# Kernel tuning notes

Hardware: AMD Instinct MI355X
Metric: run time of the kernel (lower is better)

The kernel has to match this reference:

```python
import jax, jax.numpy as jnp
import numpy as np

B, T, D = 2, 2048, 1024
K, F = 8, 4096
LAMBDA = 0.5


def setup_inputs() -> dict:
    key = jax.random.key(0)
    ks = jax.random.split(key, 8)
    s = 0.02
    return {
        "x": jax.random.normal(ks[0], (B, T, D), dtype=jnp.float32),
        "prev_logits": jax.random.normal(ks[1], (B, T, K), dtype=jnp.float32),
        "Wt": jax.random.normal(ks[2], (D, K), dtype=jnp.float32) * s,
        "Wgt": jax.random.normal(ks[3], (K, K), dtype=jnp.float32) * s,
        "We_logits": jnp.zeros((K,), dtype=jnp.float32),
        "W1": jax.random.normal(ks[4], (K, D, F), dtype=jnp.float32) * s,
        "b1": jnp.zeros((K, F), dtype=jnp.float32),
        "W2": jax.random.normal(ks[5], (K, F, D), dtype=jnp.float32) * s,
        "b2": jnp.zeros((K, D), dtype=jnp.float32),
    }


def reference(x, prev_logits, Wt, Wgt, We_logits, W1, b1, W2, b2):
    # gating: softmax over router logits, sigmoid-threshold multi-hot mask
    logits = jnp.einsum("btd,dk->btk", x, Wt) + jnp.einsum("btk,kj->btj", prev_logits, Wgt)
    st = jax.nn.softmax(logits, axis=-1)                       # (B,T,K)
    We = jax.nn.sigmoid(We_logits)                             # (K,)
    mask = (st > LAMBDA * We).astype(x.dtype)                  # (B,T,K)
    g = st * mask
    sel_counts = mask.sum(axis=(0, 1))                         # (K,)
    avg_density = mask.sum(axis=-1).mean()                     # scalar

    # dense multi-expert FFN: every expert on every token (dropout=0 / eval)
    h = jax.nn.gelu(jnp.einsum("btd,kdf->bktf", x, W1) + b1[:, None, :], approximate=False)
    outk = jnp.einsum("bktf,kfd->bktd", h, W2) + b2[:, None, :]  # (B,K,T,D)
    y = jnp.einsum("btk,bktd->btd", g, outk)
    y = y / (g.sum(axis=-1, keepdims=True) + 1e-6)
    return y, jax.lax.stop_gradient(logits), sel_counts, avg_density
```

## Files before the change

### kernel.cpp

```cpp
#include <hip/hip_runtime.h>
#include <cstdint>
#include <cstddef>

#define NB 2
#define NTT 2048
#define ND 1024
#define NK 8
#define NF 4096
#define NTOK (NB*NTT)
#define LAMBDA_C 0.5f

#define Y_SZ   (NTOK*ND)
#define LG_OFF Y_SZ
#define SC_OFF (LG_OFF + NTOK*NK)
#define AD_OFF (SC_OFF + NK)

#define WS_CNT    0
#define WS_SEG    8
#define WS_NTILES 17
#define WS_TILEK  32
#define WS_TILER  1056
#define WS_PTOK   4096
#define WS_PCOEF  36864
#define WS_COEF   69632
#define WS_X16    102400
#define B_X16   409600ull
#define B_W1T   8798208ull
#define B_W2T   75907072ull
#define B_HBUFN 143015936ull
#define B_HBUFF 8798208ull

#define BM 128
#define BN 64
#define BK 64
#define SPLITK2 4
#define KT 16

#define AOFF0 0u
#define AOFF1 16384u
#define BOFF0 32768u
#define BOFF1 40960u

typedef float  f32x4 __attribute__((ext_vector_type(4)));
typedef _Float16 f16x8 __attribute__((ext_vector_type(8)));
typedef unsigned int u32x2 __attribute__((ext_vector_type(2)));
typedef unsigned int u32x4 __attribute__((ext_vector_type(4)));

__device__ __forceinline__ unsigned int pkrtz(float a, float b){
    auto h = __builtin_amdgcn_cvt_pkrtz(a, b);
    return __builtin_bit_cast(unsigned int, h);
}
__device__ __forceinline__ float gelu_exact(float v){
    return 0.5f * v * (1.0f + erff(v * 0.70710678118654752440f));
}

__global__ __launch_bounds__(256) void k_xcast(const float* __restrict__ x,
                                               unsigned short* __restrict__ x16)
{
    int i = (blockIdx.x*256 + threadIdx.x) * 16;
    const f32x4* src = (const f32x4*)(x + i);
    f32x4 v0 = src[0], v1 = src[1], v2 = src[2], v3 = src[3];
    u32x4 o0 = {pkrtz(v0[0],v0[1]), pkrtz(v0[2],v0[3]), pkrtz(v1[0],v1[1]), pkrtz(v1[2],v1[3])};
    u32x4 o1 = {pkrtz(v2[0],v2[1]), pkrtz(v2[2],v2[3]), pkrtz(v3[0],v3[1]), pkrtz(v3[2],v3[3])};
    *(u32x4*)(x16 + i)     = o0;
    *(u32x4*)(x16 + i + 8) = o1;
}

__global__ __launch_bounds__(256) void k_wtrans(
    const float* __restrict__ W1, const float* __restrict__ W2,
    unsigned short* __restrict__ W1T, unsigned short* __restrict__ W2T)
{
    __shared__ unsigned short LT[64][72];
    int b = blockIdx.x;
    const float* src; unsigned short* dst; int sld, dld;
    if (b < 8192){
        int k = b >> 10, dt = (b >> 6) & 15, ft = b & 63;
        src = W1 + ((size_t)k*ND + dt*64)*NF + ft*64; sld = NF;
        dst = W1T + ((size_t)k*NF + ft*64)*ND + dt*64; dld = ND;
    } else {
        int b2 = b - 8192;
        int k = b2 >> 10, ft = (b2 >> 4) & 63, dt = b2 & 15;
        src = W2 + ((size_t)k*NF + ft*64)*ND + dt*64; sld = ND;
        dst = W2T + ((size_t)k*ND + dt*64)*NF + ft*64; dld = NF;
    }
    int t = threadIdx.x;
    int rg = t >> 4, cg = t & 15;
    f32x4 v[4];
    #pragma unroll
    for (int i = 0; i < 4; i++) v[i] = *(const f32x4*)(src + (size_t)(rg*4+i)*sld + cg*4);
    unsigned wA[4], wB[4];
    #pragma unroll
    for (int r = 0; r < 4; r++){
        wA[r] = pkrtz(v[r][0], v[r][1]);
        wB[r] = pkrtz(v[r][2], v[r][3]);
    }
    #pragma unroll
    for (int j = 0; j < 4; j++){
        unsigned s0 = (j < 2) ? wA[1] : wB[1];
        unsigned s1 = (j < 2) ? wA[0] : wB[0];
        unsigned s2 = (j < 2) ? wA[3] : wB[3];
        unsigned s3 = (j < 2) ? wA[2] : wB[2];
        unsigned sel = (j & 1) ? 0x07060302u : 0x05040100u;
        unsigned o0 = __builtin_amdgcn_perm(s0, s1, sel);
        unsigned o1 = __builtin_amdgcn_perm(s2, s3, sel);
        *(u32x2*)(&LT[cg*4+j][rg*4]) = (u32x2){o0, o1};
    }
    __syncthreads();
    int c = t >> 2, ch = t & 3;
    u32x4 r0 = *(const u32x4*)(&LT[c][ch*16]);
    u32x4 r1 = *(const u32x4*)(&LT[c][ch*16 + 8]);
    unsigned short* dp = dst + (size_t)c*dld + ch*16;
    *(u32x4*)(dp)     = r0;
    *(u32x4*)(dp + 8) = r1;
}

__global__ __launch_bounds__(256) void k_gating(
    const float* __restrict__ x, const float* __restrict__ pl,
    const float* __restrict__ Wt, const float* __restrict__ Wgt,
    const float* __restrict__ Wel, float* __restrict__ out,
    float* __restrict__ coef, int* __restrict__ cnt)
{
    int t = blockIdx.x;
    const float* xt = x + (size_t)t * ND;
    float acc[NK] = {0,0,0,0,0,0,0,0};
    for (int d = threadIdx.x; d < ND; d += 256){
        float xv = xt[d];
        const float4* w = (const float4*)(Wt + (size_t)d * NK);
        float4 w0 = w[0], w1 = w[1];
        acc[0] += xv*w0.x; acc[1] += xv*w0.y; acc[2] += xv*w0.z; acc[3] += xv*w0.w;
        acc[4] += xv*w1.x; acc[5] += xv*w1.y; acc[6] += xv*w1.z; acc[7] += xv*w1.w;
    }
    __shared__ float red[4][NK];
    #pragma unroll
    for (int k = 0; k < NK; k++){
        float v = acc[k];
        #pragma unroll
        for (int off = 32; off; off >>= 1) v += __shfl_down(v, off);
        if ((threadIdx.x & 63) == 0) red[threadIdx.x >> 6][k] = v;
    }
    __syncthreads();
    if (threadIdx.x == 0){
        const float* p = pl + (size_t)t * NK;
        float pv[NK];
        #pragma unroll
        for (int j = 0; j < NK; j++) pv[j] = p[j];
        float lg[NK]; float mx = -1e30f;
        #pragma unroll
        for (int k = 0; k < NK; k++){
            float v = red[0][k] + red[1][k] + red[2][k] + red[3][k];
            #pragma unroll
            for (int j = 0; j < NK; j++) v += pv[j] * Wgt[j*NK + k];
            lg[k] = v; mx = fmaxf(mx, v);
            out[LG_OFF + (size_t)t*NK + k] = v;
        }
        float e[NK]; float s = 0.f;
        #pragma unroll
        for (int k = 0; k < NK; k++){ e[k] = expf(lg[k] - mx); s += e[k]; }
        float g[NK]; float gsum = 0.f;
        #pragma unroll
        for (int k = 0; k < NK; k++){
            float st = e[k] / s;
            float we = 1.f / (1.f + expf(-Wel[k]));
            bool m = st > LAMBDA_C * we;
            g[k] = m ? st : 0.f;
            gsum += g[k];
        }
        float inv = 1.f / (gsum + 1e-6f);
        #pragma unroll
        for (int k = 0; k < NK; k++){
            coef[(size_t)t*NK + k] = g[k] * inv;
            if (g[k] > 0.f) atomicAdd(&cnt[k], 1);
        }
    }
}

__global__ __launch_bounds__(256) void k_scan(
    const float* __restrict__ coef, int* __restrict__ wsi,
    float* __restrict__ wsf, int pair_cap)
{
    int k = blockIdx.x;
    const int* cnt = wsi + WS_CNT;
    int base = 0;
    for (int j = 0; j < k; j++) base += cnt[j];
    int tid = threadIdx.x, lane = tid & 63, w = tid >> 6;
    __shared__ int wsum[4];
    __shared__ int sbase;
    if (tid == 0){
        sbase = base;
        wsi[WS_SEG + k] = base;
        if (k == NK-1) wsi[WS_SEG + NK] = base + cnt[k];
    }
    __syncthreads();
    int* ptok = wsi + WS_PTOK;
    float* pc = wsf + WS_PCOEF;
    for (int c0 = 0; c0 < NTOK; c0 += 256){
        int t = c0 + tid;
        float c = coef[(size_t)t*NK + k];
        bool m = c > 0.f;
        unsigned long long bal = __ballot(m);
        int pre = __popcll(bal & ((1ull << lane) - 1ull));
        if (lane == 0) wsum[w] = __popcll(bal);
        __syncthreads();
        int b = sbase;
        for (int j = 0; j < w; j++) b += wsum[j];
        if (m){
            int pos = b + pre;
            if (pos < pair_cap){ ptok[pos] = t; pc[pos] = c; }
        }
        __syncthreads();
        if (tid == 0) sbase += wsum[0] + wsum[1] + wsum[2] + wsum[3];
        __syncthreads();
    }
}

__global__ void k_tiles(int* __restrict__ wsi, float* __restrict__ out, int pair_cap)
{
    if (threadIdx.x == 0 && blockIdx.x == 0){
        const int* cnt = wsi + WS_CNT;
        const int* seg = wsi + WS_SEG;
        int total = 0;
        for (int k = 0; k < NK; k++){ total += cnt[k]; out[SC_OFF + k] = (float)cnt[k]; }
        out[AD_OFF] = (float)total / (float)NTOK;
        int nt = 0;
        for (int k = 0; k < NK; k++){
            int e = min(seg[k+1], pair_cap);
            for (int r = seg[k]; r < e; r += BM){
                wsi[WS_TILEK + nt] = k; wsi[WS_TILER + nt] = r; nt++;
            }
        }
        wsi[WS_NTILES] = nt;
    }
}

#define XCD_PART_LOOP(nwork)                                              \
    int q_ = (nwork) >> 3, rr_ = (nwork) & 7;                             \
    int xcd_ = blockIdx.x & 7;                                            \
    int slot_ = blockIdx.x >> 3;                                          \
    int nslot_ = gridDim.x >> 3;                                          \
    int cntw_ = q_ + (xcd_ < rr_ ? 1 : 0);                                \
    int start_ = xcd_ * q_ + (xcd_ < rr_ ? xcd_ : rr_);                   \
    for (int p_ = slot_; p_ < cntw_; p_ += nslot_)


#define GLLN(aP0_, aP1_, bP0_, bP1_, t_, slot_)                           \
  { unsigned ab_ = (unsigned)(slot_)*16384u + (unsigned)(wv*1024);        \
    __builtin_amdgcn_global_load_lds(                                     \
        (const __attribute__((address_space(1))) void*)((aP0_) + (size_t)(t_)*32), \
        (__attribute__((address_space(3))) void*)(&lds[ab_]), 16, 0, 0);  \
    __builtin_amdgcn_global_load_lds(                                     \
        (const __attribute__((address_space(1))) void*)((aP1_) + (size_t)(t_)*32), \
        (__attribute__((address_space(3))) void*)(&lds[ab_ + 4096u]), 16, 0, 0); \
    __builtin_amdgcn_global_load_lds(                                     \
        (const __attribute__((address_space(1))) void*)((bP0_) + (size_t)(t_)*32), \
        (__attribute__((address_space(3))) void*)(&lds[ab_ + 8192u]), 16, 0, 0); \
    __builtin_amdgcn_global_load_lds(                                     \
        (const __attribute__((address_space(1))) void*)((bP1_) + (size_t)(t_)*32), \
        (__attribute__((address_space(3))) void*)(&lds[ab_ + 12288u]), 16, 0, 0); }

#define MFMAN(slot_)                                                      \
  { unsigned ab_ = (unsigned)(slot_)*16384u, bb_ = ab_ + 8192u;           \
    f16x8 af_[4], bf_[4];                                                 \
    _Pragma("unroll")                                                     \
    for (int m_ = 0; m_ < 4; m_++) af_[m_] = *(const f16x8*)(&lds[ab_ + aoff[m_]]); \
    _Pragma("unroll")                                                     \
    for (int n_ = 0; n_ < 4; n_++) bf_[n_] = *(const f16x8*)(&lds[bb_ + boff[n_]]); \
    __builtin_amdgcn_s_setprio(1);                                        \
    _Pragma("unroll")                                                     \
    for (int m_ = 0; m_ < 4; m_++)                                        \
    _Pragma("unroll")                                                     \
    for (int n_ = 0; n_ < 4; n_++)                                        \
        acc[m_][n_] = __builtin_amdgcn_mfma_f32_16x16x32_f16(af_[m_], bf_[n_], acc[m_][n_], 0, 0, 0); \
    __builtin_amdgcn_s_setprio(0); }

#define GEMMN_PRE()                                                       \
    int tid = threadIdx.x;                                                \
    int L = tid & 63;                                                     \
    int wv = tid >> 6;                                                    \
    int wr = wv >> 1, wc = wv & 1;                                        \
    int l15 = L & 15, q = L >> 4;                                         \
    unsigned aoff[4], boff[4];                                            \
    _Pragma("unroll")                                                     \
    for (int m_ = 0; m_ < 4; m_++){                                       \
        int r_ = wr*64 + m_*16 + l15;                                     \
        aoff[m_] = (unsigned)(r_*64) + ((unsigned)((q ^ r_) & 3) << 4);   \
    }                                                                     \
    _Pragma("unroll")                                                     \
    for (int n_ = 0; n_ < 4; n_++){                                       \
        int c_ = wc*64 + n_*16 + l15;                                     \
        boff[n_] = (unsigned)(c_*64) + ((unsigned)((q ^ c_) & 3) << 4);   \
    }                                                                     \
    int grow0 = wv*16 + (L >> 2);                                         \
    int grow1 = (4 + wv)*16 + (L >> 2);                                   \
    int qg8 = (((L & 3) ^ ((L >> 2) & 3))) * 8;

__global__ __launch_bounds__(256, 4) void k_gemm1n(
    const unsigned short* __restrict__ x16, const unsigned short* __restrict__ w1t,
    const float* __restrict__ b1, const int* __restrict__ wsi,
    unsigned short* __restrict__ hbuf, int pair_cap)
{
    __shared__ char lds[32768];
    __shared__ int stok[BM];
    const int* seg  = wsi + WS_SEG;
    const int* tk   = wsi + WS_TILEK;
    const int* tr   = wsi + WS_TILER;
    const int* ptok = wsi + WS_PTOK;
    int ntm = wsi[WS_NTILES];
    int nwork = ntm * (NF / 128);
    GEMMN_PRE()

    XCD_PART_LOOP(nwork){
        int widx = start_ + p_;
        int mt = widx % ntm;
        int ft = widx / ntm;
        int kexp = tk[mt];
        int row0 = tr[mt];
        int nrows = min(BM, seg[kexp+1] - row0);
        int f0 = ft * 128;
        __syncthreads();
        if (tid < BM){
            int r = row0 + tid;
            stok[tid] = (tid < nrows && r < pair_cap) ? ptok[r] : ptok[row0];
        }
        __syncthreads();
        const unsigned short* a0 = x16 + (size_t)stok[grow0]*ND + qg8;
        const unsigned short* a1 = x16 + (size_t)stok[grow1]*ND + qg8;
        const unsigned short* bb = w1t + (size_t)kexp*NF*ND;
        const unsigned short* b0 = bb + (size_t)(f0 + grow0)*ND + qg8;
        const unsigned short* b1p = bb + (size_t)(f0 + grow1)*ND + qg8;
        f32x4 acc[4][4] = {};
        GLLN(a0, a1, b0, b1p, 0, 0)
        __syncthreads();
        for (int t = 0; t < 32; t++){
            if (t + 1 < 32){ GLLN(a0, a1, b0, b1p, t+1, (t+1)&1) }
            MFMAN(t & 1)
            __syncthreads();
        }
        const float* b1k = b1 + (size_t)kexp*NF;
        #pragma unroll
        for (int n = 0; n < 4; n++){
            int f = f0 + wc*64 + n*16 + l15;
            float bv = b1k[f];
            #pragma unroll
            for (int m = 0; m < 4; m++){
                int rl = wr*64 + m*16 + q*4;
                #pragma unroll
                for (int i = 0; i < 4; i++){
                    int r = rl + i;
                    if (r < nrows && row0 + r < pair_cap){
                        float v = gelu_exact(acc[m][n][i] + bv);
                        hbuf[(size_t)(row0+r)*NF + f] = (unsigned short)(pkrtz(v, 0.f) & 0xffffu);
                    }
                }
            }
        }
    }
}

__global__ __launch_bounds__(256, 4) void k_gemm2n(
    const unsigned short* __restrict__ hbuf, const unsigned short* __restrict__ w2t,
    const float* __restrict__ b2, const int* __restrict__ wsi,
    const float* __restrict__ wsf, float* __restrict__ out, int pair_cap)
{
    __shared__ char lds[32768];
    __shared__ int stok[BM];
    __shared__ float scoef[BM];
    const int* seg  = wsi + WS_SEG;
    const int* tk   = wsi + WS_TILEK;
    const int* tr   = wsi + WS_TILER;
    const int* ptok = wsi + WS_PTOK;
    const float* pcoef = wsf + WS_PCOEF;
    int ntm = wsi[WS_NTILES];
    int nwork = ntm * (ND / 128) * SPLITK2;
    GEMMN_PRE()

    XCD_PART_LOOP(nwork){
        int widx = start_ + p_;
        int mt = widx % ntm;
        int rest = widx / ntm;
        int dt = rest & 7;
        int spk = rest >> 3;
        int kexp = tk[mt];
        int row0 = tr[mt];
        int nrows = min(BM, seg[kexp+1] - row0);
        int d0 = dt * 128;
        __syncthreads();
        if (tid < BM){
            int r = row0 + tid;
            bool v = (tid < nrows && r < pair_cap);
            stok[tid]  = v ? ptok[r] : 0;
            scoef[tid] = v ? pcoef[r] : 0.f;
        }
        __syncthreads();
        int ar0 = row0 + grow0; if (ar0 >= pair_cap) ar0 = pair_cap - 1;
        int ar1 = row0 + grow1; if (ar1 >= pair_cap) ar1 = pair_cap - 1;
        const unsigned short* a0 = hbuf + (size_t)ar0*NF + spk*(NF/SPLITK2) + qg8;
        const unsigned short* a1 = hbuf + (size_t)ar1*NF + spk*(NF/SPLITK2) + qg8;
        const unsigned short* bb = w2t + (size_t)kexp*ND*NF + spk*(NF/SPLITK2);
        const unsigned short* b0 = bb + (size_t)(d0 + grow0)*NF + qg8;
        const unsigned short* b1p = bb + (size_t)(d0 + grow1)*NF + qg8;
        f32x4 acc[4][4] = {};
        GLLN(a0, a1, b0, b1p, 0, 0)
        __syncthreads();
        for (int t = 0; t < 32; t++){
            if (t + 1 < 32){ GLLN(a0, a1, b0, b1p, t+1, (t+1)&1) }
            MFMAN(t & 1)
            __syncthreads();
        }
        const float* b2k = b2 + (size_t)kexp*ND;
        #pragma unroll
        for (int n = 0; n < 4; n++){
            int d = d0 + wc*64 + n*16 + l15;
            float bv = (spk == 0) ? b2k[d] : 0.f;
            #pragma unroll
            for (int m = 0; m < 4; m++){
                int rl = wr*64 + m*16 + q*4;
                #pragma unroll
                for (int i = 0; i < 4; i++){
                    int r = rl + i;
                    if (r < nrows && row0 + r < pair_cap){
                        float c = scoef[r];
                        atomicAdd(&out[(size_t)stok[r]*ND + d], c * (acc[m][n][i] + bv));
                    }
                }
            }
        }
    }
}

#define LOAD_A(dst_, tt_)                                                 \
    { const unsigned short* an_ = asrc + (tt_)*BK;                        \
      _Pragma("unroll")                                                   \
      for (int j_ = 0; j_ < 4; j_++) dst_[j_] = *(const u32x4*)(an_ + j_*8); }

#define LOAD_B(dst_, tt_, LDW_)                                           \
    { const float* bn_ = bsrc + (size_t)((tt_)*BK + bkq*4)*LDW_;          \
      _Pragma("unroll")                                                   \
      for (int r_ = 0; r_ < 4; r_++) dst_[r_] = *(const f32x4*)(bn_ + (size_t)r_*LDW_); }

#define STAGE_A(src_, AO_)                                                \
    { _Pragma("unroll")                                                   \
      for (int j_ = 0; j_ < 4; j_++){                                     \
          unsigned off_ = (AO_) + (unsigned)arow*128u +                   \
              ((((unsigned)(ahalf*4 + j_)) ^ (unsigned)(arow & 7)) << 4); \
          *(u32x4*)(&lds[off_]) = src_[j_];                               \
      } }

#define STAGE_B(src_, BO_)                                                \
    { unsigned wA_[4], wB_[4];                                            \
      _Pragma("unroll")                                                   \
      for (int r_ = 0; r_ < 4; r_++){                                     \
          wA_[r_] = pkrtz(src_[r_][0], src_[r_][1]);                      \
          wB_[r_] = pkrtz(src_[r_][2], src_[r_][3]);                      \
      }                                                                   \
      _Pragma("unroll")                                                   \
      for (int j_ = 0; j_ < 4; j_++){                                     \
          unsigned s0_ = (j_ < 2) ? wA_[1] : wB_[1];                      \
          unsigned s1_ = (j_ < 2) ? wA_[0] : wB_[0];                      \
          unsigned s2_ = (j_ < 2) ? wA_[3] : wB_[3];                      \
          unsigned s3_ = (j_ < 2) ? wA_[2] : wB_[2];                      \
          unsigned sel_ = (j_ & 1) ? 0x07060302u : 0x05040100u;           \
          unsigned o0_ = __builtin_amdgcn_perm(s0_, s1_, sel_);           \
          unsigned o1_ = __builtin_amdgcn_perm(s2_, s3_, sel_);           \
          unsigned col_ = (unsigned)(bcc*4 + j_);                         \
          unsigned off_ = (BO_) + col_*128u +                             \
              (((unsigned)(bkq*8)) ^ ((col_ & 7u) << 4));                 \
          *(u32x2*)(&lds[off_]) = (u32x2){o0_, o1_};                      \
      } }

#define MFMA_RD(AO_, BO_)                                                 \
    { __builtin_amdgcn_s_setprio(1);                                      \
      _Pragma("unroll")                                                   \
      for (int kk_ = 0; kk_ < 2; kk_++){                                  \
          unsigned sb_ = ((unsigned)(kk_*64 + q*16)) ^ swzL;              \
          f16x8 af_[4], bf_[2];                                           \
          _Pragma("unroll")                                               \
          for (int m_ = 0; m_ < 4; m_++)                                  \
              af_[m_] = *(const f16x8*)(&lds[(AO_) + (unsigned)(wr*64 + m_*16 + l15)*128u + sb_]); \
          _Pragma("unroll")                                               \
          for (int n_ = 0; n_ < 2; n_++)                                  \
              bf_[n_] = *(const f16x8*)(&lds[(BO_) + (unsigned)(wc*32 + n_*16 + l15)*128u + sb_]); \
          _Pragma("unroll")                                               \
          for (int m_ = 0; m_ < 4; m_++)                                  \
          _Pragma("unroll")                                               \
          for (int n_ = 0; n_ < 2; n_++)                                  \
              acc[m_][n_] = __builtin_amdgcn_mfma_f32_16x16x32_f16(af_[m_], bf_[n_], acc[m_][n_], 0, 0, 0); \
      }                                                                   \
      __builtin_amdgcn_s_setprio(0); }

#define STEP_SYNC()                                                       \
    asm volatile("s_waitcnt lgkmcnt(0)" ::: "memory");                    \
    __builtin_amdgcn_s_barrier();                                         \
    __builtin_amdgcn_sched_barrier(0);

__global__ __launch_bounds__(256, 3) void k_gemm1f(
    const unsigned short* __restrict__ x16, const float* __restrict__ W1,
    const float* __restrict__ b1, const int* __restrict__ wsi,
    unsigned short* __restrict__ hbuf, int pair_cap)
{
    __shared__ char lds[49152];
    __shared__ int stok[BM];
    const int* seg  = wsi + WS_SEG;
    const int* tk   = wsi + WS_TILEK;
    const int* tr   = wsi + WS_TILER;
    const int* ptok = wsi + WS_PTOK;
    int ntm = wsi[WS_NTILES];
    int nwork = ntm * (NF / BN);
    int tid  = threadIdx.x;
    int lane = tid & 63;
    int w    = tid >> 6;
    int wr = w >> 1, wc = w & 1;
    int l15 = lane & 15, q = lane >> 4;
    unsigned swzL = (unsigned)((l15 & 7) << 4);
    int arow = tid >> 1, ahalf = tid & 1;
    int bkq = tid >> 4, bcc = tid & 15;

    XCD_PART_LOOP(nwork){
        int widx = start_ + p_;
        int mt = widx % ntm;
        int ft = widx / ntm;
        int kexp = tk[mt];
        int row0 = tr[mt];
        int nrows = min(BM, seg[kexp+1] - row0);
        int f0 = ft * BN;
        __syncthreads();
        if (tid < BM){
            int r = row0 + tid;
            stok[tid] = (tid < nrows && r < pair_cap) ? ptok[r] : ptok[row0];
        }
        __syncthreads();
        const unsigned short* asrc = x16 + (size_t)stok[arow]*ND + ahalf*32;
        const float* bsrc = W1 + (size_t)kexp*ND*NF + f0 + bcc*4;
        u32x4 ga0[4], ga1[4]; f32x4 gb0[4], gb1[4];
        LOAD_A(ga0, 0) LOAD_B(gb0, 0, NF)
        LOAD_A(ga1, 1) LOAD_B(gb1, 1, NF)
        f32x4 acc[4][2] = {};
        for (int t = 0; t < KT; t += 2){
            STAGE_A(ga0, AOFF0) STAGE_B(gb0, BOFF0)
            if (t + 2 < KT){ LOAD_A(ga0, t+2) LOAD_B(gb0, t+2, NF) }
            STEP_SYNC()
            MFMA_RD(AOFF0, BOFF0)
            STAGE_A(ga1, AOFF1) STAGE_B(gb1, BOFF1)
            if (t + 3 < KT){ LOAD_A(ga1, t+3) LOAD_B(gb1, t+3, NF) }
            STEP_SYNC()
            MFMA_RD(AOFF1, BOFF1)
        }
        const float* b1k = b1 + (size_t)kexp*NF;
        #pragma unroll
        for (int n = 0; n < 2; n++){
            int f = f0 + wc*32 + n*16 + l15;
            float bv = b1k[f];
            #pragma unroll
            for (int m = 0; m < 4; m++){
                int rl = wr*64 + m*16 + q*4;
                #pragma unroll
                for (int i = 0; i < 4; i++){
                    int r = rl + i;
                    if (r < nrows && row0 + r < pair_cap){
                        float v = gelu_exact(acc[m][n][i] + bv);
                        hbuf[(size_t)(row0+r)*NF + f] = (unsigned short)(pkrtz(v, 0.f) & 0xffffu);
                    }
                }
            }
        }
    }
}

__global__ __launch_bounds__(256, 3) void k_gemm2f(
    const unsigned short* __restrict__ hbuf, const float* __restrict__ W2,
    const float* __restrict__ b2, const int* __restrict__ wsi,
    const float* __restrict__ wsf, float* __restrict__ out, int pair_cap)
{
    __shared__ char lds[49152];
    __shared__ int stok[BM];
    __shared__ float scoef[BM];
    const int* seg  = wsi + WS_SEG;
    const int* tk   = wsi + WS_TILEK;
    const int* tr   = wsi + WS_TILER;
    const int* ptok = wsi + WS_PTOK;
    const float* pcoef = wsf + WS_PCOEF;
    int ntm = wsi[WS_NTILES];
    int nwork = ntm * (ND / BN) * SPLITK2;
    int tid  = threadIdx.x;
    int lane = tid & 63;
    int w    = tid >> 6;
    int wr = w >> 1, wc = w & 1;
    int l15 = lane & 15, q = lane >> 4;
    unsigned swzL = (unsigned)((l15 & 7) << 4);
    int arow = tid >> 1, ahalf = tid & 1;
    int bkq = tid >> 4, bcc = tid & 15;

    XCD_PART_LOOP(nwork){
        int widx = start_ + p_;
        int mt = widx % ntm;
        int rest = widx / ntm;
        int dt = rest & 15;
        int sp = rest >> 4;
        int kexp = tk[mt];
        int row0 = tr[mt];
        int nrows = min(BM, seg[kexp+1] - row0);
        int d0 = dt * BN;
        __syncthreads();
        if (tid < BM){
            int r = row0 + tid;
            bool v = (tid < nrows && r < pair_cap);
            stok[tid]  = v ? ptok[r] : 0;
            scoef[tid] = v ? pcoef[r] : 0.f;
        }
        __syncthreads();
        int hr = row0 + arow; if (hr >= pair_cap) hr = pair_cap - 1;
        const unsigned short* asrc = hbuf + (size_t)hr*NF + sp*(NF/SPLITK2) + ahalf*32;
        const float* bsrc = W2 + (size_t)kexp*NF*ND + (size_t)sp*(NF/SPLITK2)*ND + d0 + bcc*4;
        u32x4 ga0[4], ga1[4]; f32x4 gb0[4], gb1[4];
        LOAD_A(ga0, 0) LOAD_B(gb0, 0, ND)
        LOAD_A(ga1, 1) LOAD_B(gb1, 1, ND)
        f32x4 acc[4][2] = {};
        for (int t = 0; t < KT; t += 2){
            STAGE_A(ga0, AOFF0) STAGE_B(gb0, BOFF0)
            if (t + 2 < KT){ LOAD_A(ga0, t+2) LOAD_B(gb0, t+2, ND) }
            STEP_SYNC()
            MFMA_RD(AOFF0, BOFF0)
            STAGE_A(ga1, AOFF1) STAGE_B(gb1, BOFF1)
            if (t + 3 < KT){ LOAD_A(ga1, t+3) LOAD_B(gb1, t+3, ND) }
            STEP_SYNC()
            MFMA_RD(AOFF1, BOFF1)
        }
        const float* b2k = b2 + (size_t)kexp*ND;
        #pragma unroll
        for (int n = 0; n < 2; n++){
            int d = d0 + wc*32 + n*16 + l15;
            float bv = (sp == 0) ? b2k[d] : 0.f;
            #pragma unroll
            for (int m = 0; m < 4; m++){
                int rl = wr*64 + m*16 + q*4;
                #pragma unroll
                for (int i = 0; i < 4; i++){
                    int r = rl + i;
                    if (r < nrows && row0 + r < pair_cap){
                        float c = scoef[r];
                        atomicAdd(&out[(size_t)stok[r]*ND + d], c * (acc[m][n][i] + bv));
                    }
                }
            }
        }
    }
}

extern "C" void kernel_launch(void* const* d_in, const int* in_sizes, int n_in,
                              void* d_out, int out_size, void* d_ws, size_t ws_size,
                              hipStream_t stream)
{
    const float* x   = (const float*)d_in[0];
    const float* pl  = (const float*)d_in[1];
    const float* Wt  = (const float*)d_in[2];
    const float* Wgt = (const float*)d_in[3];
    const float* Wel = (const float*)d_in[4];
    const float* W1  = (const float*)d_in[5];
    const float* b1  = (const float*)d_in[6];
    const float* W2  = (const float*)d_in[7];
    const float* b2  = (const float*)d_in[8];
    float* out = (float*)d_out;
    int* wsi   = (int*)d_ws;
    float* wsf = (float*)d_ws;
    unsigned short* x16 = (unsigned short*)((char*)d_ws + B_X16);

    long long capn = ((long long)ws_size - (long long)B_HBUFN) / ((long long)NF*2);
    bool newpath = capn >= 4096;

    hipMemsetAsync(d_out, 0, (size_t)out_size*sizeof(float), stream);
    hipMemsetAsync(d_ws, 0, 32, stream);
    k_xcast<<<1024, 256, 0, stream>>>(x, x16);
    k_gating<<<NTOK, 256, 0, stream>>>(x, pl, Wt, Wgt, Wel, out, wsf + WS_COEF, wsi + WS_CNT);

    if (newpath){
        unsigned short* w1t  = (unsigned short*)((char*)d_ws + B_W1T);
        unsigned short* w2t  = (unsigned short*)((char*)d_ws + B_W2T);
        unsigned short* hbuf = (unsigned short*)((char*)d_ws + B_HBUFN);
        int pair_cap = (int)((capn > 32768) ? 32768 : capn);
        k_wtrans<<<16384, 256, 0, stream>>>(W1, W2, w1t, w2t);
        k_scan<<<NK, 256, 0, stream>>>(wsf + WS_COEF, wsi, wsf, pair_cap);
        k_tiles<<<1, 64, 0, stream>>>(wsi, out, pair_cap);
        k_gemm1n<<<2048, 256, 0, stream>>>(x16, w1t, b1, wsi, hbuf, pair_cap);
        k_gemm2n<<<2048, 256, 0, stream>>>(hbuf, w2t, b2, wsi, wsf, out, pair_cap);
    } else {
        unsigned short* hbuf = (unsigned short*)((char*)d_ws + B_HBUFF);
        long long cap = ((long long)ws_size - (long long)B_HBUFF) / ((long long)NF*2);
        if (cap > (long long)NTOK*NK) cap = (long long)NTOK*NK;
        if (cap < 0) cap = 0;
        int pair_cap = (int)cap;
        if (pair_cap > 0){
            k_scan<<<NK, 256, 0, stream>>>(wsf + WS_COEF, wsi, wsf, pair_cap);
            k_tiles<<<1, 64, 0, stream>>>(wsi, out, pair_cap);
            k_gemm1f<<<2048, 256, 0, stream>>>(x16, W1, b1, wsi, hbuf, pair_cap);
            k_gemm2f<<<2048, 256, 0, stream>>>(hbuf, W2, b2, wsi, wsf, out, pair_cap);
        }
    }
}
```

Measured before the change: 269.9 us.

## Triple-buffer GEMM LDS pipeline with vmcnt waits and swizzle weight-transpose LDS

Both grouped expert GEMMs move from a double-buffered global_load_lds loop with a full __syncthreads per step to a three-slot ring. Loads run two K-steps ahead, and a partial s_waitcnt vmcnt plus a raw s_barrier replaces the full sync, so more global latency is hidden behind MFMA work. LDS per block grows from 32 to 48 KB, and launch bounds drop from 4 to 3 blocks per CU. Separately, the weight-transpose kernel replaces its padded LDS tile with an XOR-swizzled layout to avoid bank conflicts.

```diff
diff --git a/kernel.cpp b/kernel.cpp
--- a/kernel.cpp
+++ b/kernel.cpp
@@ -70,7 +70,7 @@
     const float* __restrict__ W1, const float* __restrict__ W2,
     unsigned short* __restrict__ W1T, unsigned short* __restrict__ W2T)
 {
-    __shared__ unsigned short LT[64][72];
+    __shared__ char LT[8192];
     int b = blockIdx.x;
     const float* src; unsigned short* dst; int sld, dld;
     if (b < 8192){
@@ -103,12 +103,17 @@
         unsigned sel = (j & 1) ? 0x07060302u : 0x05040100u;
         unsigned o0 = __builtin_amdgcn_perm(s0, s1, sel);
         unsigned o1 = __builtin_amdgcn_perm(s2, s3, sel);
-        *(u32x2*)(&LT[cg*4+j][rg*4]) = (u32x2){o0, o1};
+        unsigned row_ = (unsigned)(cg*4 + j);
+        unsigned g_ = ((unsigned)rg) ^ (2u*(row_ & 7u));
+        *(u32x2*)(&LT[row_*128u + g_*8u]) = (u32x2){o0, o1};
     }
     __syncthreads();
     int c = t >> 2, ch = t & 3;
-    u32x4 r0 = *(const u32x4*)(&LT[c][ch*16]);
-    u32x4 r1 = *(const u32x4*)(&LT[c][ch*16 + 8]);
+    unsigned sfx = (unsigned)c & 7u;
+    unsigned p0 = ((unsigned)(2*ch))     ^ sfx;
+    unsigned p1 = ((unsigned)(2*ch + 1)) ^ sfx;
+    u32x4 r0 = *(const u32x4*)(&LT[(unsigned)c*128u + p0*16u]);
+    u32x4 r1 = *(const u32x4*)(&LT[(unsigned)c*128u + p1*16u]);
     unsigned short* dp = dst + (size_t)c*dld + ch*16;
     *(u32x4*)(dp)     = r0;
     *(u32x4*)(dp + 8) = r1;
@@ -271,6 +276,30 @@
     for (int n_ = 0; n_ < 4; n_++)                                        \
         acc[m_][n_] = __builtin_amdgcn_mfma_f32_16x16x32_f16(af_[m_], bf_[n_], acc[m_][n_], 0, 0, 0); \
     __builtin_amdgcn_s_setprio(0); }
+
+#define PIPE_N(APREF0_, APREF1_, BPREF0_, BPREF1_)                        \
+    GLLN(APREF0_, APREF1_, BPREF0_, BPREF1_, 0, 0)                        \
+    GLLN(APREF0_, APREF1_, BPREF0_, BPREF1_, 1, 1)                        \
+    asm volatile("s_waitcnt vmcnt(4)" ::: "memory");                      \
+    __builtin_amdgcn_s_barrier();                                         \
+    __builtin_amdgcn_sched_barrier(0);                                    \
+    for (int t = 0; t < 32; t++){                                         \
+        int sl = t % 3;                                                   \
+        if (t + 2 < 32){                                                  \
+            GLLN(APREF0_, APREF1_, BPREF0_, BPREF1_, t+2, (t+2)%3)        \
+            MFMAN(sl)                                                     \
+            asm volatile("s_waitcnt vmcnt(4)" ::: "memory");              \
+            __builtin_amdgcn_s_barrier();                                 \
+            __builtin_amdgcn_sched_barrier(0);                            \
+        } else if (t + 1 < 32){                                           \
+            MFMAN(sl)                                                     \
+            asm volatile("s_waitcnt vmcnt(0)" ::: "memory");              \
+            __builtin_amdgcn_s_barrier();                                 \
+            __builtin_amdgcn_sched_barrier(0);                            \
+        } else {                                                          \
+            MFMAN(sl)                                                     \
+        }                                                                 \
+    }
 
 #define GEMMN_PRE()                                                       \
     int tid = threadIdx.x;                                                \
@@ -293,12 +322,12 @@
     int grow1 = (4 + wv)*16 + (L >> 2);                                   \
     int qg8 = (((L & 3) ^ ((L >> 2) & 3))) * 8;
 
-__global__ __launch_bounds__(256, 4) void k_gemm1n(
+__global__ __launch_bounds__(256, 3) void k_gemm1n(
     const unsigned short* __restrict__ x16, const unsigned short* __restrict__ w1t,
     const float* __restrict__ b1, const int* __restrict__ wsi,
     unsigned short* __restrict__ hbuf, int pair_cap)
 {
-    __shared__ char lds[32768];
+    __shared__ char lds[49152];
     __shared__ int stok[BM];
     const int* seg  = wsi + WS_SEG;
     const int* tk   = wsi + WS_TILEK;
@@ -328,13 +357,7 @@
         const unsigned short* b0 = bb + (size_t)(f0 + grow0)*ND + qg8;
         const unsigned short* b1p = bb + (size_t)(f0 + grow1)*ND + qg8;
         f32x4 acc[4][4] = {};
-        GLLN(a0, a1, b0, b1p, 0, 0)
-        __syncthreads();
-        for (int t = 0; t < 32; t++){
-            if (t + 1 < 32){ GLLN(a0, a1, b0, b1p, t+1, (t+1)&1) }
-            MFMAN(t & 1)
-            __syncthreads();
-        }
+        PIPE_N(a0, a1, b0, b1p)
         const float* b1k = b1 + (size_t)kexp*NF;
         #pragma unroll
         for (int n = 0; n < 4; n++){
@@ -356,12 +379,12 @@
     }
 }
 
-__global__ __launch_bounds__(256, 4) void k_gemm2n(
+__global__ __launch_bounds__(256, 3) void k_gemm2n(
     const unsigned short* __restrict__ hbuf, const unsigned short* __restrict__ w2t,
     const float* __restrict__ b2, const int* __restrict__ wsi,
     const float* __restrict__ wsf, float* __restrict__ out, int pair_cap)
 {
-    __shared__ char lds[32768];
+    __shared__ char lds[49152];
     __shared__ int stok[BM];
     __shared__ float scoef[BM];
     const int* seg  = wsi + WS_SEG;
@@ -399,13 +422,7 @@
         const unsigned short* b0 = bb + (size_t)(d0 + grow0)*NF + qg8;
         const unsigned short* b1p = bb + (size_t)(d0 + grow1)*NF + qg8;
         f32x4 acc[4][4] = {};
-        GLLN(a0, a1, b0, b1p, 0, 0)
-        __syncthreads();
-        for (int t = 0; t < 32; t++){
-            if (t + 1 < 32){ GLLN(a0, a1, b0, b1p, t+1, (t+1)&1) }
-            MFMAN(t & 1)
-            __syncthreads();
-        }
+        PIPE_N(a0, a1, b0, b1p)
         const float* b2k = b2 + (size_t)kexp*ND;
         #pragma unroll
         for (int n = 0; n < 4; n++){
```

New measurement: 270.2 us. About the same (+0.1%).
